# Kernel optimization log

Hardware: AMD Instinct MI355X
Metric: run time of the kernel (lower is better)

Reference implementation:

```python
import jax, jax.numpy as jnp
import numpy as np

NUM_HEADS = 16
D_MODEL = 1024
NEG_INF = -1e30


def setup_inputs() -> dict:
    key = jax.random.key(0)
    ks = jax.random.split(key, 7)
    B, S, D = 2, 2048, D_MODEL
    scale = 1.0 / np.sqrt(D)
    return {
        "queries": jax.random.normal(ks[0], (B, S, D), dtype=jnp.float32),
        "keys": jax.random.normal(ks[1], (B, S, D), dtype=jnp.float32),
        "values": jax.random.normal(ks[2], (B, S, D), dtype=jnp.float32),
        "Wq": jax.random.normal(ks[3], (D, D), dtype=jnp.float32) * scale,
        "Wk": jax.random.normal(ks[4], (D, D), dtype=jnp.float32) * scale,
        "Wv": jax.random.normal(ks[5], (D, D), dtype=jnp.float32) * scale,
        "Wo": jax.random.normal(ks[6], (D, D), dtype=jnp.float32) * scale,
    }


def _split_heads(x, h):
    # [B, S, D] -> [B, h, S, D/h]
    B, S, D = x.shape
    return x.reshape(B, S, h, D // h).transpose(0, 2, 1, 3)


def reference(queries, keys, values, Wq, Wk, Wv, Wo):
    h = NUM_HEADS
    q = _split_heads(queries @ Wq, h)  # [B, h, S, dh]
    k = _split_heads(keys @ Wk, h)
    v = _split_heads(values @ Wv, h)
    dh = q.shape[-1]
    scores = jnp.einsum("bhqd,bhkd->bhqk", q, k) / jnp.sqrt(jnp.float32(dh))
    # original quirk: exactly-zero scores are masked to -1e30 before softmax
    scores = jnp.where(scores == 0, NEG_INF, scores)
    attn = jax.nn.softmax(scores, axis=-1)
    out = jnp.einsum("bhqk,bhkd->bhqd", attn, v)  # [B, h, S, dh]
    B, _, S, _ = out.shape
    out = out.transpose(0, 2, 1, 3).reshape(B, S, h * dh)
    return out @ Wo
```

## Files before the change

kernel.cpp:

```cpp
#include <hip/hip_runtime.h>

typedef unsigned short u16;
typedef short bf16x8 __attribute__((ext_vector_type(8)));
typedef float f32x4 __attribute__((ext_vector_type(4)));

namespace {

constexpr int kB = 2, kS = 2048, kD = 1024, kH = 16, kDh = 64;
constexpr float kC2 = 0.125f * 1.44269504088896341f;

__device__ inline u16 f32_bf16(float f) {
    unsigned u = __float_as_uint(f);
    u += 0x7FFFu + ((u >> 16) & 1u);
    return (u16)(u >> 16);
}

__device__ inline u16 f32_bf16_fast(float f) {
    return (u16)((__float_as_uint(f) + 0x8000u) >> 16);
}

__device__ inline float fast_exp2(float x) {
    float r;
    asm("v_exp_f32 %0, %1" : "=v"(r) : "v"(x));
    return r;
}

__device__ inline void gl_lds16(const void* g, void* l) {
    __builtin_amdgcn_global_load_lds(
        (const __attribute__((address_space(1))) void*)g,
        (__attribute__((address_space(3))) void*)l, 16, 0, 0);
}

__device__ inline int swz8(int l) {
    return ((l & 3) ^ ((l >> 2) & 3) ^ ((l >> 4) & 3)) * 8;
}

__global__ __launch_bounds__(256) void conv_bf16_3(
    const float* __restrict__ s0, const float* __restrict__ s1,
    const float* __restrict__ s2,
    u16* __restrict__ d0, u16* __restrict__ d1, u16* __restrict__ d2)
{
    const int z = blockIdx.y;
    const float* src = z == 0 ? s0 : (z == 1 ? s1 : s2);
    u16* dst = z == 0 ? d0 : (z == 1 ? d1 : d2);
    const int i = blockIdx.x * 256 + threadIdx.x;
    const float4* s4 = (const float4*)src;
    float4 a = s4[2 * i], b = s4[2 * i + 1];
    uint4 o;
    o.x = (unsigned)f32_bf16(a.x) | ((unsigned)f32_bf16(a.y) << 16);
    o.y = (unsigned)f32_bf16(a.z) | ((unsigned)f32_bf16(a.w) << 16);
    o.z = (unsigned)f32_bf16(b.x) | ((unsigned)f32_bf16(b.y) << 16);
    o.w = (unsigned)f32_bf16(b.z) | ((unsigned)f32_bf16(b.w) << 16);
    ((uint4*)dst)[i] = o;
}

__global__ __launch_bounds__(256) void wtrans4(
    const float* __restrict__ W0, const float* __restrict__ W1,
    const float* __restrict__ W2, const float* __restrict__ W3,
    u16* __restrict__ T0, u16* __restrict__ T1,
    u16* __restrict__ T2, u16* __restrict__ T3)
{
    const int z = blockIdx.z;
    const float* W = z == 0 ? W0 : (z == 1 ? W1 : (z == 2 ? W2 : W3));
    u16* Wt = z == 0 ? T0 : (z == 1 ? T1 : (z == 2 ? T2 : T3));
    const float sc = (z == 0) ? kC2 : 1.0f;

    __shared__ __attribute__((aligned(16))) u16 T[64][65];
    const int t = threadIdx.x;
    const int n0 = blockIdx.x * 64, k0 = blockIdx.y * 64;
    const int r = t >> 4, c4 = (t & 15) * 4;
#pragma unroll
    for (int it = 0; it < 4; ++it) {
        const int rr = r + 16 * it;
        float4 v = *(const float4*)(W + (size_t)(k0 + rr) * kD + n0 + c4);
        T[rr][c4 + 0] = f32_bf16(v.x * sc);
        T[rr][c4 + 1] = f32_bf16(v.y * sc);
        T[rr][c4 + 2] = f32_bf16(v.z * sc);
        T[rr][c4 + 3] = f32_bf16(v.w * sc);
    }
    __syncthreads();
#pragma unroll
    for (int it = 0; it < 4; ++it) {
        const int nn = r + 16 * it;
        uint2 pk;
        pk.x = (unsigned)T[c4 + 0][nn] | ((unsigned)T[c4 + 1][nn] << 16);
        pk.y = (unsigned)T[c4 + 2][nn] | ((unsigned)T[c4 + 3][nn] << 16);
        *(uint2*)(Wt + (size_t)(n0 + nn) * kD + k0 + c4) = pk;
    }
}

__global__ __launch_bounds__(256) void vtrans(
    const u16* __restrict__ V, u16* __restrict__ Vt)
{
    __shared__ __attribute__((aligned(16))) u16 T[64][65];
    const int t = threadIdx.x;
    const int s0 = blockIdx.x * 64;
    const int bh = blockIdx.y, b = bh >> 4, h = bh & 15;
    const int rr = t >> 3, c0 = (t & 7) * 8;
    union { u16 u[8]; uint4 v4; } buf;
#pragma unroll
    for (int p = 0; p < 2; ++p) {
        const int s = rr + 32 * p;
        buf.v4 = *(const uint4*)(V + (size_t)(b * kS + s0 + s) * kD + h * kDh + c0);
#pragma unroll
        for (int i = 0; i < 8; ++i) T[c0 + i][s] = buf.u[i];
    }
    __syncthreads();
#pragma unroll
    for (int p = 0; p < 2; ++p) {
        const int d = rr + 32 * p;
#pragma unroll
        for (int i = 0; i < 8; ++i) buf.u[i] = T[d][c0 + i];
        *(uint4*)(Vt + (size_t)(bh * kDh + d) * kS + s0 + c0) = buf.v4;
    }
}

template <bool F32OUT>
__device__ inline void gemm128_body(
    const u16* __restrict__ A, const u16* __restrict__ Wt,
    void* __restrict__ Cout, int M, int N, int K, int bx, int by)
{
    __shared__ __attribute__((aligned(16))) u16 As[128 * 32];
    __shared__ __attribute__((aligned(16))) u16 Bs[128 * 32];
    const int t = threadIdx.x, w = t >> 6, l = t & 63;
    const int quad = l >> 4, c = l & 15;
    const int wm = w >> 1, wn = w & 1;
    const int m0 = by * 128, n0 = bx * 128;
    const int lr = l >> 2, lc = swz8(l);
    const int xc = ((quad ^ (c & 3) ^ ((c >> 2) & 3))) * 8;

    const u16* ga0 = A  + (size_t)(m0 + w * 32 + lr) * K + lc;
    const u16* ga1 = A  + (size_t)(m0 + w * 32 + 16 + lr) * K + lc;
    const u16* gb0 = Wt + (size_t)(n0 + w * 32 + lr) * K + lc;
    const u16* gb1 = Wt + (size_t)(n0 + w * 32 + 16 + lr) * K + lc;
    u16* la0 = &As[(w * 32) * 32];
    u16* la1 = &As[(w * 32 + 16) * 32];
    u16* lb0 = &Bs[(w * 32) * 32];
    u16* lb1 = &Bs[(w * 32 + 16) * 32];

    f32x4 acc[4][4];
#pragma unroll
    for (int mi = 0; mi < 4; ++mi)
#pragma unroll
        for (int nj = 0; nj < 4; ++nj) acc[mi][nj] = 0;

    for (int k0 = 0; k0 < K; k0 += 32) {
        gl_lds16(ga0 + k0, la0);
        gl_lds16(ga1 + k0, la1);
        gl_lds16(gb0 + k0, lb0);
        gl_lds16(gb1 + k0, lb1);
        __syncthreads();
        bf16x8 af[4], bf[4];
#pragma unroll
        for (int mi = 0; mi < 4; ++mi)
            af[mi] = *(const bf16x8*)&As[(wm * 64 + mi * 16 + c) * 32 + xc];
#pragma unroll
        for (int nj = 0; nj < 4; ++nj)
            bf[nj] = *(const bf16x8*)&Bs[(wn * 64 + nj * 16 + c) * 32 + xc];
#pragma unroll
        for (int mi = 0; mi < 4; ++mi)
#pragma unroll
            for (int nj = 0; nj < 4; ++nj)
                acc[mi][nj] = __builtin_amdgcn_mfma_f32_16x16x32_bf16(
                    af[mi], bf[nj], acc[mi][nj], 0, 0, 0);
        __syncthreads();
    }

#pragma unroll
    for (int mi = 0; mi < 4; ++mi)
#pragma unroll
        for (int nj = 0; nj < 4; ++nj)
#pragma unroll
            for (int r = 0; r < 4; ++r) {
                const size_t row = m0 + wm * 64 + mi * 16 + quad * 4 + r;
                const size_t col = n0 + wn * 64 + nj * 16 + c;
                if (F32OUT)
                    ((float*)Cout)[row * N + col] = acc[mi][nj][r];
                else
                    ((u16*)Cout)[row * N + col] = f32_bf16(acc[mi][nj][r]);
            }
}

__global__ __launch_bounds__(256) void gemm_qkv(
    const u16* __restrict__ A0, const u16* __restrict__ A1,
    const u16* __restrict__ A2,
    const u16* __restrict__ W0, const u16* __restrict__ W1,
    const u16* __restrict__ W2,
    u16* __restrict__ C0, u16* __restrict__ C1, u16* __restrict__ C2)
{
    const int z = blockIdx.z;
    const u16* A  = z == 0 ? A0 : (z == 1 ? A1 : A2);
    const u16* Wt = z == 0 ? W0 : (z == 1 ? W1 : W2);
    u16* C = z == 0 ? C0 : (z == 1 ? C1 : C2);
    gemm128_body<false>(A, Wt, C, kB * kS, kD, kD, blockIdx.x, blockIdx.y);
}

__global__ __launch_bounds__(256) void gemm_out(
    const u16* __restrict__ A, const u16* __restrict__ Wt,
    float* __restrict__ C)
{
    gemm128_body<true>(A, Wt, C, kB * kS, kD, kD, blockIdx.x, blockIdx.y);
}

__global__ __launch_bounds__(256) void attn(
    const u16* __restrict__ Q, const u16* __restrict__ K,
    const u16* __restrict__ Vt, u16* __restrict__ AO)
{
    __shared__ __attribute__((aligned(16))) u16 KsL[2 * 64 * 32];
    __shared__ __attribute__((aligned(16))) u16 VtL[2 * 64 * 32];
    __shared__ __attribute__((aligned(16))) u16 Qs[2 * 64 * 32];
    __shared__ __attribute__((aligned(16))) u16 Ps[4 * 16 * 72];

    const int t = threadIdx.x, w = t >> 6, l = t & 63;
    const int quad = l >> 4, c = l & 15;
    const int q0 = blockIdx.x * 64;
    const int bh = blockIdx.y, b = bh >> 4, h = bh & 15;
    const int lr = l >> 2, lc8 = swz8(l);
    const int xc = ((quad ^ (c & 3) ^ ((c >> 2) & 3))) * 8;

    const size_t qbase = (size_t)(b * kS + q0) * kD + h * kDh;
#pragma unroll
    for (int p = 0; p < 2; ++p)
        gl_lds16(Q + qbase + (size_t)(w * 16 + lr) * kD + p * 32 + lc8,
                 &Qs[p * 2048 + (w * 16) * 32]);
    __syncthreads();

    bf16x8 qf[2];
#pragma unroll
    for (int p = 0; p < 2; ++p)
        qf[p] = *(const bf16x8*)&Qs[p * 2048 + (w * 16 + c) * 32 + xc];

    bf16x8 ones;
#pragma unroll
    for (int i = 0; i < 8; ++i) ones[i] = (short)0x3F80;

    f32x4 o[4], ol;
#pragma unroll
    for (int nj = 0; nj < 4; ++nj) o[nj] = 0;
    ol = 0;

    const size_t kbase = (size_t)(b * kS) * kD + h * kDh;
    const size_t vbase = (size_t)bh * kDh * kS;
    const int p_w = w >> 1, hf_w = w & 1;

    for (int kt = 0; kt < kS / 64; ++kt) {
#pragma unroll
        for (int h2 = 0; h2 < 2; ++h2) {
            const int r0 = hf_w * 32 + h2 * 16;
            gl_lds16(K + kbase + (size_t)(kt * 64 + r0 + lr) * kD + p_w * 32 + lc8,
                     &KsL[p_w * 2048 + r0 * 32]);
            gl_lds16(Vt + vbase + (size_t)(r0 + lr) * kS + kt * 64 + p_w * 32 + lc8,
                     &VtL[p_w * 2048 + r0 * 32]);
        }
        __syncthreads();

        f32x4 s[4];
#pragma unroll
        for (int nj = 0; nj < 4; ++nj) s[nj] = 0;
#pragma unroll
        for (int p = 0; p < 2; ++p) {
#pragma unroll
            for (int nj = 0; nj < 4; ++nj) {
                const bf16x8 bk =
                    *(const bf16x8*)&KsL[p * 2048 + (nj * 16 + c) * 32 + xc];
                s[nj] = __builtin_amdgcn_mfma_f32_16x16x32_bf16(
                    qf[p], bk, s[nj], 0, 0, 0);
            }
        }

#pragma unroll
        for (int nj = 0; nj < 4; ++nj)
#pragma unroll
            for (int r = 0; r < 4; ++r) {
                const float p = fast_exp2(s[nj][r]);
                Ps[w * 1152 + (quad * 4 + r) * 72 + nj * 16 + c] = f32_bf16_fast(p);
            }

#pragma unroll
        for (int kp = 0; kp < 2; ++kp) {
            const bf16x8 pf =
                *(const bf16x8*)&Ps[w * 1152 + c * 72 + kp * 32 + quad * 8];
#pragma unroll
            for (int nj = 0; nj < 4; ++nj) {
                const bf16x8 vf =
                    *(const bf16x8*)&VtL[kp * 2048 + (nj * 16 + c) * 32 + xc];
                o[nj] = __builtin_amdgcn_mfma_f32_16x16x32_bf16(
                    pf, vf, o[nj], 0, 0, 0);
            }
            ol = __builtin_amdgcn_mfma_f32_16x16x32_bf16(pf, ones, ol, 0, 0, 0);
        }
        __syncthreads();
    }

    const size_t obase = (size_t)(b * kS + q0 + w * 16) * kD + h * kDh;
#pragma unroll
    for (int r = 0; r < 4; ++r) {
        const float inv = 1.0f / ol[r];
#pragma unroll
        for (int nj = 0; nj < 4; ++nj)
            AO[obase + (size_t)(quad * 4 + r) * kD + nj * 16 + c] =
                f32_bf16(o[nj][r] * inv);
    }
}

}

extern "C" void kernel_launch(void* const* d_in, const int* in_sizes, int n_in,
                              void* d_out, int out_size, void* d_ws, size_t ws_size,
                              hipStream_t stream)
{
    const float* q_in = (const float*)d_in[0];
    const float* k_in = (const float*)d_in[1];
    const float* v_in = (const float*)d_in[2];
    const float* Wq   = (const float*)d_in[3];
    const float* Wk   = (const float*)d_in[4];
    const float* Wv   = (const float*)d_in[5];
    const float* Wo   = (const float*)d_in[6];

    u16* ws = (u16*)d_ws;
    const size_t M1 = 1u << 20;
    u16* xq  = ws;
    u16* xk  = ws + 4 * M1;
    u16* xv  = ws + 8 * M1;
    u16* Wtq = ws + 12 * M1;
    u16* Wtk = ws + 13 * M1;
    u16* Wtv = ws + 14 * M1;
    u16* Wto = ws + 15 * M1;
    u16* Qp  = ws + 16 * M1;
    u16* Kp  = ws + 20 * M1;
    u16* Vp  = ws + 24 * M1;
    u16* AO  = ws + 28 * M1;
    u16* Vtg = xq;

    hipLaunchKernelGGL(conv_bf16_3, dim3(2048, 3), dim3(256), 0, stream,
                       q_in, k_in, v_in, xq, xk, xv);

    hipLaunchKernelGGL(wtrans4, dim3(16, 16, 4), dim3(256), 0, stream,
                       Wq, Wk, Wv, Wo, Wtq, Wtk, Wtv, Wto);

    hipLaunchKernelGGL(gemm_qkv, dim3(8, 32, 3), dim3(256), 0, stream,
                       xq, xk, xv, Wtq, Wtk, Wtv, Qp, Kp, Vp);

    hipLaunchKernelGGL(vtrans, dim3(32, 32), dim3(256), 0, stream, Vp, Vtg);

    hipLaunchKernelGGL(attn, dim3(32, 32), dim3(256), 0, stream, Qp, Kp, Vtg, AO);

    hipLaunchKernelGGL(gemm_out, dim3(8, 32), dim3(256), 0, stream,
                       AO, Wto, (float*)d_out);
}
```

Baseline: 249.3 us.

## Switch attention to 32x32 MFMA tiles with 128-query blocks

Rewrites the attention kernel so each wave handles 32 query rows using 32x32x16 bf16 MFMAs instead of 16x16x32. Each block now covers 128 queries, which halves the grid and doubles reuse of each loaded K/V tile. LDS layouts move to 64-wide rows with an XOR swizzle. The intent is to cut global K/V traffic and per-MFMA overhead, at the cost of more accumulator registers and fewer blocks to fill the GPU (512 blocks).

```diff
diff --git a/kernel.cpp b/kernel.cpp
--- a/kernel.cpp
+++ b/kernel.cpp
@@ -3,6 +3,7 @@
 typedef unsigned short u16;
 typedef short bf16x8 __attribute__((ext_vector_type(8)));
 typedef float f32x4 __attribute__((ext_vector_type(4)));
+typedef float f32x16 __attribute__((ext_vector_type(16)));
 
 namespace {
 
@@ -206,100 +207,98 @@
     const u16* __restrict__ Q, const u16* __restrict__ K,
     const u16* __restrict__ Vt, u16* __restrict__ AO)
 {
-    __shared__ __attribute__((aligned(16))) u16 KsL[2 * 64 * 32];
-    __shared__ __attribute__((aligned(16))) u16 VtL[2 * 64 * 32];
-    __shared__ __attribute__((aligned(16))) u16 Qs[2 * 64 * 32];
-    __shared__ __attribute__((aligned(16))) u16 Ps[4 * 16 * 72];
+    __shared__ __attribute__((aligned(16))) u16 KsL[64 * 64];
+    __shared__ __attribute__((aligned(16))) u16 VtL[64 * 64];
+    __shared__ __attribute__((aligned(16))) u16 Qs[4 * 32 * 64];
+    __shared__ __attribute__((aligned(16))) u16 Ps[4 * 32 * 64];
 
     const int t = threadIdx.x, w = t >> 6, l = t & 63;
-    const int quad = l >> 4, c = l & 15;
-    const int q0 = blockIdx.x * 64;
+    const int half = l >> 5, m = l & 31;
+    const int q0 = blockIdx.x * 128;
     const int bh = blockIdx.y, b = bh >> 4, h = bh & 15;
-    const int lr = l >> 2, lc8 = swz8(l);
-    const int xc = ((quad ^ (c & 3) ^ ((c >> 2) & 3))) * 8;
-
-    const size_t qbase = (size_t)(b * kS + q0) * kD + h * kDh;
-#pragma unroll
-    for (int p = 0; p < 2; ++p)
-        gl_lds16(Q + qbase + (size_t)(w * 16 + lr) * kD + p * 32 + lc8,
-                 &Qs[p * 2048 + (w * 16) * 32]);
+    const int sl = l >> 3;
+    const int sc = (l & 7) ^ sl;
+
+    const size_t qbase = (size_t)(b * kS + q0 + w * 32) * kD + h * kDh;
+#pragma unroll
+    for (int i = 0; i < 4; ++i)
+        gl_lds16(Q + qbase + (size_t)(i * 8 + sl) * kD + sc * 8,
+                 &Qs[w * 2048 + i * 512]);
     __syncthreads();
 
-    bf16x8 qf[2];
-#pragma unroll
-    for (int p = 0; p < 2; ++p)
-        qf[p] = *(const bf16x8*)&Qs[p * 2048 + (w * 16 + c) * 32 + xc];
+    bf16x8 qf[4];
+#pragma unroll
+    for (int ch = 0; ch < 4; ++ch)
+        qf[ch] = *(const bf16x8*)
+            &Qs[w * 2048 + m * 64 + ((2 * ch + half) ^ (m & 7)) * 8];
 
     bf16x8 ones;
 #pragma unroll
     for (int i = 0; i < 8; ++i) ones[i] = (short)0x3F80;
 
-    f32x4 o[4], ol;
-#pragma unroll
-    for (int nj = 0; nj < 4; ++nj) o[nj] = 0;
-    ol = 0;
+    f32x16 o0 = 0, o1 = 0, ol = 0;
 
     const size_t kbase = (size_t)(b * kS) * kD + h * kDh;
     const size_t vbase = (size_t)bh * kDh * kS;
-    const int p_w = w >> 1, hf_w = w & 1;
 
     for (int kt = 0; kt < kS / 64; ++kt) {
 #pragma unroll
-        for (int h2 = 0; h2 < 2; ++h2) {
-            const int r0 = hf_w * 32 + h2 * 16;
-            gl_lds16(K + kbase + (size_t)(kt * 64 + r0 + lr) * kD + p_w * 32 + lc8,
-                     &KsL[p_w * 2048 + r0 * 32]);
-            gl_lds16(Vt + vbase + (size_t)(r0 + lr) * kS + kt * 64 + p_w * 32 + lc8,
-                     &VtL[p_w * 2048 + r0 * 32]);
+        for (int i = 0; i < 2; ++i) {
+            const int R0 = w * 16 + i * 8;
+            gl_lds16(K + kbase + (size_t)(kt * 64 + R0 + sl) * kD + sc * 8,
+                     &KsL[R0 * 64]);
+            gl_lds16(Vt + vbase + (size_t)(R0 + sl) * kS + kt * 64 + sc * 8,
+                     &VtL[R0 * 64]);
         }
         __syncthreads();
 
-        f32x4 s[4];
-#pragma unroll
-        for (int nj = 0; nj < 4; ++nj) s[nj] = 0;
-#pragma unroll
-        for (int p = 0; p < 2; ++p) {
-#pragma unroll
-            for (int nj = 0; nj < 4; ++nj) {
-                const bf16x8 bk =
-                    *(const bf16x8*)&KsL[p * 2048 + (nj * 16 + c) * 32 + xc];
-                s[nj] = __builtin_amdgcn_mfma_f32_16x16x32_bf16(
-                    qf[p], bk, s[nj], 0, 0, 0);
+        f32x16 s0 = 0, s1 = 0;
+#pragma unroll
+        for (int ch = 0; ch < 4; ++ch) {
+            const int xo = ((2 * ch + half) ^ (m & 7)) * 8;
+            const bf16x8 kf0 = *(const bf16x8*)&KsL[(m) * 64 + xo];
+            const bf16x8 kf1 = *(const bf16x8*)&KsL[(32 + m) * 64 + xo];
+            s0 = __builtin_amdgcn_mfma_f32_32x32x16_bf16(qf[ch], kf0, s0, 0, 0, 0);
+            s1 = __builtin_amdgcn_mfma_f32_32x32x16_bf16(qf[ch], kf1, s1, 0, 0, 0);
+        }
+
+#pragma unroll
+        for (int reg = 0; reg < 16; ++reg) {
+            const int qrow = (reg & 3) + 8 * (reg >> 2) + 4 * half;
+            const int base = w * 2048 + qrow * 64;
+            const int sw = (qrow & 7);
+            {
+                const int key = m;
+                Ps[base + ((key >> 3) ^ sw) * 8 + (key & 7)] =
+                    f32_bf16_fast(fast_exp2(s0[reg]));
+            }
+            {
+                const int key = 32 + m;
+                Ps[base + ((key >> 3) ^ sw) * 8 + (key & 7)] =
+                    f32_bf16_fast(fast_exp2(s1[reg]));
             }
         }
 
 #pragma unroll
-        for (int nj = 0; nj < 4; ++nj)
-#pragma unroll
-            for (int r = 0; r < 4; ++r) {
-                const float p = fast_exp2(s[nj][r]);
-                Ps[w * 1152 + (quad * 4 + r) * 72 + nj * 16 + c] = f32_bf16_fast(p);
-            }
-
-#pragma unroll
-        for (int kp = 0; kp < 2; ++kp) {
-            const bf16x8 pf =
-                *(const bf16x8*)&Ps[w * 1152 + c * 72 + kp * 32 + quad * 8];
-#pragma unroll
-            for (int nj = 0; nj < 4; ++nj) {
-                const bf16x8 vf =
-                    *(const bf16x8*)&VtL[kp * 2048 + (nj * 16 + c) * 32 + xc];
-                o[nj] = __builtin_amdgcn_mfma_f32_16x16x32_bf16(
-                    pf, vf, o[nj], 0, 0, 0);
-            }
-            ol = __builtin_amdgcn_mfma_f32_16x16x32_bf16(pf, ones, ol, 0, 0, 0);
+        for (int ch = 0; ch < 4; ++ch) {
+            const int xo = ((2 * ch + half) ^ (m & 7)) * 8;
+            const bf16x8 pf = *(const bf16x8*)&Ps[w * 2048 + m * 64 + xo];
+            const bf16x8 vf0 = *(const bf16x8*)&VtL[(m) * 64 + xo];
+            const bf16x8 vf1 = *(const bf16x8*)&VtL[(32 + m) * 64 + xo];
+            o0 = __builtin_amdgcn_mfma_f32_32x32x16_bf16(pf, vf0, o0, 0, 0, 0);
+            o1 = __builtin_amdgcn_mfma_f32_32x32x16_bf16(pf, vf1, o1, 0, 0, 0);
+            ol = __builtin_amdgcn_mfma_f32_32x32x16_bf16(pf, ones, ol, 0, 0, 0);
         }
         __syncthreads();
     }
 
-    const size_t obase = (size_t)(b * kS + q0 + w * 16) * kD + h * kDh;
-#pragma unroll
-    for (int r = 0; r < 4; ++r) {
-        const float inv = 1.0f / ol[r];
-#pragma unroll
-        for (int nj = 0; nj < 4; ++nj)
-            AO[obase + (size_t)(quad * 4 + r) * kD + nj * 16 + c] =
-                f32_bf16(o[nj][r] * inv);
+    const size_t obase = (size_t)(b * kS + q0 + w * 32) * kD + h * kDh;
+#pragma unroll
+    for (int reg = 0; reg < 16; ++reg) {
+        const int qrow = (reg & 3) + 8 * (reg >> 2) + 4 * half;
+        const float inv = 1.0f / ol[reg];
+        AO[obase + (size_t)qrow * kD + m]      = f32_bf16(o0[reg] * inv);
+        AO[obase + (size_t)qrow * kD + 32 + m] = f32_bf16(o1[reg] * inv);
     }
 }
 
@@ -343,7 +342,7 @@
 
     hipLaunchKernelGGL(vtrans, dim3(32, 32), dim3(256), 0, stream, Vp, Vtg);
 
-    hipLaunchKernelGGL(attn, dim3(32, 32), dim3(256), 0, stream, Qp, Kp, Vtg, AO);
+    hipLaunchKernelGGL(attn, dim3(16, 32), dim3(256), 0, stream, Qp, Kp, Vtg, AO);
 
     hipLaunchKernelGGL(gemm_out, dim3(8, 32), dim3(256), 0, stream,
                        AO, Wto, (float*)d_out);
```

After: 244.4 us. No clear change (-2.0%).
